# Performance work log

Hardware: AMD Instinct MI355X
Metric: run time of the kernel (lower is better)

The kernel has to match this reference:

```python
import jax, jax.numpy as jnp
import numpy as np

N, F, E, C = 50000, 128, 800000, 2

def setup_inputs() -> dict:
    key = jax.random.key(0)
    k1, k2, k3, k4, k5, k6 = jax.random.split(key, 6)
    x = jax.random.normal(k1, (N, F), dtype=jnp.float32)
    edge_index = jax.random.randint(k2, (2, E), 0, N, dtype=jnp.int64)
    s_node = 1.0 / np.sqrt(F)
    s_edge = 1.0 / np.sqrt(2 * F)
    W_node = jax.random.uniform(k3, (C, F), jnp.float32, -s_node, s_node)
    b_node = jax.random.uniform(k4, (C,), jnp.float32, -s_node, s_node)
    W_edge = jax.random.uniform(k5, (C * C, 2 * F), jnp.float32, -s_edge, s_edge)
    b_edge = jax.random.uniform(k6, (C * C,), jnp.float32, -s_edge, s_edge)
    return {"x": x, "edge_index": edge_index, "W_node": W_node, "b_node": b_node,
            "W_edge": W_edge, "b_edge": b_edge}

def reference(x, edge_index, W_node, b_node, W_edge, b_edge):
    # node potentials: [N, C]
    node_pot = x @ W_node.T + b_node
    # gather endpoint features: u, v are [E, F]
    u = x[edge_index[0]]
    v = x[edge_index[1]]
    # concat(u, v) @ W_edge.T == u @ W_edge[:, :F].T + v @ W_edge[:, F:].T
    # (avoids materializing the [E, 2F] concat)
    edge_pot = u @ W_edge[:, :x.shape[1]].T + v @ W_edge[:, x.shape[1]:].T + b_edge
    return node_pot, edge_pot
```

## Files before the change

kernel.cpp:

```cpp
#include <hip/hip_runtime.h>

#define F 128

__global__ void detect_idx64(const int* __restrict__ ei, int* __restrict__ flag) {
    if (blockIdx.x == 0 && threadIdx.x == 0) {
        int orv = 0;
#pragma unroll
        for (int k = 0; k < 16; ++k) orv |= ei[2 * k + 1];
        *flag = (orv == 0) ? 1 : 0;
    }
}

__global__ __launch_bounds__(128) void node_pass(
    const float* __restrict__ x,
    const float* __restrict__ W_node,
    const float* __restrict__ b_node,
    const float* __restrict__ W_edge,
    const float* __restrict__ b_edge,
    float2* __restrict__ node_pot,
    float4* __restrict__ pu,
    float4* __restrict__ pv,
    int n_nodes)
{
    __shared__ float w[10][F];
    __shared__ float bias[6];
    const int t = threadIdx.x;
    for (int i = t; i < 10 * F; i += 128) {
        const int r = i >> 7, k = i & (F - 1);
        float val;
        if (r < 2)      val = W_node[r * F + k];
        else if (r < 6) val = W_edge[(r - 2) * 2 * F + k];
        else            val = W_edge[(r - 6) * 2 * F + F + k];
        w[r][k] = val;
    }
    if (t < 2)      bias[t] = b_node[t];
    else if (t < 6) bias[t] = b_edge[t - 2];
    __syncthreads();

    const int n = blockIdx.x * 128 + t;
    if (n >= n_nodes) return;

    const float4* xr = (const float4*)(x + (size_t)n * F);
    float acc[10];
#pragma unroll
    for (int r = 0; r < 10; ++r) acc[r] = 0.f;

#pragma unroll
    for (int i = 0; i < F / 4; ++i) {
        const float4 xv = xr[i];
#pragma unroll
        for (int r = 0; r < 10; ++r) {
            const float4 wv = *(const float4*)&w[r][i * 4];
            acc[r] += xv.x * wv.x + xv.y * wv.y + xv.z * wv.z + xv.w * wv.w;
        }
    }

    node_pot[n] = make_float2(acc[0] + bias[0], acc[1] + bias[1]);
    pu[n] = make_float4(acc[2] + bias[2], acc[3] + bias[3],
                        acc[4] + bias[4], acc[5] + bias[5]);
    pv[n] = make_float4(acc[6], acc[7], acc[8], acc[9]);
}

__global__ __launch_bounds__(256) void edge_pass(
    const int* __restrict__ ei,
    const int* __restrict__ idx64_flag,
    const float4* __restrict__ pu,
    const float4* __restrict__ pv,
    float4* __restrict__ edge_pot,
    int n_edges)
{
    const int e = blockIdx.x * 256 + threadIdx.x;
    if (e >= n_edges) return;
    const int mode = *idx64_flag;
    int u, v;
    if (mode) {
        u = ei[2 * (size_t)e];
        v = ei[2 * ((size_t)n_edges + e)];
    } else {
        u = ei[e];
        v = ei[n_edges + e];
    }
    const float4 a = pu[u];
    const float4 b = pv[v];
    edge_pot[e] = make_float4(a.x + b.x, a.y + b.y, a.z + b.z, a.w + b.w);
}

extern "C" void kernel_launch(void* const* d_in, const int* in_sizes, int n_in,
                              void* d_out, int out_size, void* d_ws, size_t ws_size,
                              hipStream_t stream) {
    const float* x      = (const float*)d_in[0];
    const int*   ei     = (const int*)d_in[1];
    const float* W_node = (const float*)d_in[2];
    const float* b_node = (const float*)d_in[3];
    const float* W_edge = (const float*)d_in[4];
    const float* b_edge = (const float*)d_in[5];

    const int n_nodes = in_sizes[0] / F;
    const int n_edges = in_sizes[1] / 2;

    float4* pu = (float4*)d_ws;
    float4* pv = pu + n_nodes;
    int* idx64_flag = (int*)(pv + n_nodes);

    float* out = (float*)d_out;
    float2* node_pot = (float2*)out;
    float4* edge_pot = (float4*)(out + (size_t)2 * n_nodes);

    hipLaunchKernelGGL(detect_idx64, dim3(1), dim3(64), 0, stream, ei, idx64_flag);

    const int nb1 = (n_nodes + 127) / 128;
    hipLaunchKernelGGL(node_pass, dim3(nb1), dim3(128), 0, stream,
                       x, W_node, b_node, W_edge, b_edge, node_pot, pu, pv, n_nodes);

    const int nb2 = (n_edges + 255) / 256;
    hipLaunchKernelGGL(edge_pass, dim3(nb2), dim3(256), 0, stream,
                       ei, idx64_flag, pu, pv, edge_pot, n_edges);
}
```

Before: 103.3 us.

## Split node projections across four lanes and inline index-width detection

The node pass now assigns four lanes to each node. Each lane reads an interleaved quarter of the row, so the x reads are more coalesced and there are four times as many threads. Partial sums are combined with xor shuffles, and only lane 0 writes the outputs. The separate detect_idx64 launch is removed; each edge thread instead checks four odd words of the index array to decide between 32- and 64-bit indices, which drops one kernel launch but adds a few redundant broadcast loads per thread.

```diff
diff --git a/kernel.cpp b/kernel.cpp
--- a/kernel.cpp
+++ b/kernel.cpp
@@ -2,16 +2,7 @@
 
 #define F 128
 
-__global__ void detect_idx64(const int* __restrict__ ei, int* __restrict__ flag) {
-    if (blockIdx.x == 0 && threadIdx.x == 0) {
-        int orv = 0;
-#pragma unroll
-        for (int k = 0; k < 16; ++k) orv |= ei[2 * k + 1];
-        *flag = (orv == 0) ? 1 : 0;
-    }
-}
-
-__global__ __launch_bounds__(128) void node_pass(
+__global__ __launch_bounds__(256) void node_pass(
     const float* __restrict__ x,
     const float* __restrict__ W_node,
     const float* __restrict__ b_node,
@@ -25,7 +16,7 @@
     __shared__ float w[10][F];
     __shared__ float bias[6];
     const int t = threadIdx.x;
-    for (int i = t; i < 10 * F; i += 128) {
+    for (int i = t; i < 10 * F; i += 256) {
         const int r = i >> 7, k = i & (F - 1);
         float val;
         if (r < 2)      val = W_node[r * F + k];
@@ -37,33 +28,39 @@
     else if (t < 6) bias[t] = b_edge[t - 2];
     __syncthreads();
 
-    const int n = blockIdx.x * 128 + t;
-    if (n >= n_nodes) return;
+    const int quad = (blockIdx.x * 256 + t) >> 2;
+    const int j = t & 3;
+    if (quad >= n_nodes) return;
 
-    const float4* xr = (const float4*)(x + (size_t)n * F);
+    const float4* xr = (const float4*)(x + (size_t)quad * F);
     float acc[10];
 #pragma unroll
     for (int r = 0; r < 10; ++r) acc[r] = 0.f;
 
 #pragma unroll
-    for (int i = 0; i < F / 4; ++i) {
-        const float4 xv = xr[i];
+    for (int i = 0; i < 8; ++i) {
+        const float4 xv = xr[i * 4 + j];
 #pragma unroll
         for (int r = 0; r < 10; ++r) {
-            const float4 wv = *(const float4*)&w[r][i * 4];
+            const float4 wv = *(const float4*)&w[r][i * 16 + j * 4];
             acc[r] += xv.x * wv.x + xv.y * wv.y + xv.z * wv.z + xv.w * wv.w;
         }
     }
-
-    node_pot[n] = make_float2(acc[0] + bias[0], acc[1] + bias[1]);
-    pu[n] = make_float4(acc[2] + bias[2], acc[3] + bias[3],
-                        acc[4] + bias[4], acc[5] + bias[5]);
-    pv[n] = make_float4(acc[6], acc[7], acc[8], acc[9]);
+#pragma unroll
+    for (int r = 0; r < 10; ++r) {
+        acc[r] += __shfl_xor(acc[r], 1);
+        acc[r] += __shfl_xor(acc[r], 2);
+    }
+    if (j == 0) {
+        node_pot[quad] = make_float2(acc[0] + bias[0], acc[1] + bias[1]);
+        pu[quad] = make_float4(acc[2] + bias[2], acc[3] + bias[3],
+                               acc[4] + bias[4], acc[5] + bias[5]);
+        pv[quad] = make_float4(acc[6], acc[7], acc[8], acc[9]);
+    }
 }
 
 __global__ __launch_bounds__(256) void edge_pass(
     const int* __restrict__ ei,
-    const int* __restrict__ idx64_flag,
     const float4* __restrict__ pu,
     const float4* __restrict__ pv,
     float4* __restrict__ edge_pot,
@@ -71,11 +68,12 @@
 {
     const int e = blockIdx.x * 256 + threadIdx.x;
     if (e >= n_edges) return;
-    const int mode = *idx64_flag;
+    const bool idx64 = ((ei[1] | ei[3] | ei[5] | ei[7]) == 0);
     int u, v;
-    if (mode) {
-        u = ei[2 * (size_t)e];
-        v = ei[2 * ((size_t)n_edges + e)];
+    if (idx64) {
+        const int2* ei64 = (const int2*)ei;
+        u = ei64[(size_t)e].x;
+        v = ei64[(size_t)n_edges + e].x;
     } else {
         u = ei[e];
         v = ei[n_edges + e];
@@ -100,19 +98,16 @@
 
     float4* pu = (float4*)d_ws;
     float4* pv = pu + n_nodes;
-    int* idx64_flag = (int*)(pv + n_nodes);
 
     float* out = (float*)d_out;
     float2* node_pot = (float2*)out;
     float4* edge_pot = (float4*)(out + (size_t)2 * n_nodes);
 
-    hipLaunchKernelGGL(detect_idx64, dim3(1), dim3(64), 0, stream, ei, idx64_flag);
-
-    const int nb1 = (n_nodes + 127) / 128;
-    hipLaunchKernelGGL(node_pass, dim3(nb1), dim3(128), 0, stream,
+    const int nb1 = (n_nodes * 4 + 255) / 256;
+    hipLaunchKernelGGL(node_pass, dim3(nb1), dim3(256), 0, stream,
                        x, W_node, b_node, W_edge, b_edge, node_pot, pu, pv, n_nodes);
 
     const int nb2 = (n_edges + 255) / 256;
     hipLaunchKernelGGL(edge_pass, dim3(nb2), dim3(256), 0, stream,
-                       ei, idx64_flag, pu, pv, edge_pot, n_edges);
+                       ei, pu, pv, edge_pot, n_edges);
 }
```

After: 97.89 us. -5.3%, faster.
